# Kernel tuning notes

Hardware: AMD Instinct MI355X
Metric: run time of the kernel (lower is better)

The kernel has to match this reference:

```python
import jax, jax.numpy as jnp
import numpy as np

N, C, H, W = 8, 256, 128, 128
HD = 256          # hidden_depth
FC, FS, CS = 8, 2, 8  # heads_count, fold_size, center_size
EPS_GN = 1e-5


def setup_inputs() -> dict:
    key = jax.random.key(0)
    ks = jax.random.split(key, 8)
    d = {
        'x': jax.random.normal(ks[0], (N, C, H, W), jnp.float32),
        'proj_w': jax.random.normal(ks[1], (2 * HD, C), jnp.float32) * 0.02,
        'proj_b': jnp.zeros((2 * HD,), jnp.float32),
        'merge_w': jax.random.normal(ks[2], (C, HD), jnp.float32) * 0.02,
        'merge_b': jnp.zeros((C,), jnp.float32),
        'alpha': jnp.ones((1,), jnp.float32),
        'beta': jnp.zeros((1,), jnp.float32),
        'g0_w': jnp.ones((C,), jnp.float32),
        'g0_b': jnp.zeros((C,), jnp.float32),
        'mlp_w0': jax.random.normal(ks[3], (2 * C, 2 * C), jnp.float32) * 0.02,
        'mlp_b0': jnp.zeros((2 * C,), jnp.float32),
        'mlp_w1': jax.random.normal(ks[4], (2 * C, C), jnp.float32) * 0.02,
        'mlp_b1': jnp.zeros((C,), jnp.float32),
        'g1_w': jnp.ones((C,), jnp.float32),
        'g1_b': jnp.zeros((C,), jnp.float32),
        'layer_scale': jnp.full((C,), 1e-5, jnp.float32),
    }
    return d


def _group_norm1(x, w, b):
    # GroupNorm(1, C): normalize over (C,H,W) per sample, per-channel affine
    mu = x.mean(axis=(1, 2, 3), keepdims=True)
    var = ((x - mu) ** 2).mean(axis=(1, 2, 3), keepdims=True)
    xn = (x - mu) * jax.lax.rsqrt(var + EPS_GN)
    return xn * w[None, :, None, None] + b[None, :, None, None]


def _l2norm(v):
    return v / jnp.maximum(jnp.linalg.norm(v, axis=-1, keepdims=True), 1e-12)


def _local_cluster(x, proj_w, proj_b, merge_w, merge_b, alpha, beta):
    n = x.shape[0]
    # 1x1 conv proj: C -> 2*HD
    y = jnp.einsum('nchw,oc->nohw', x, proj_w) + proj_b[None, :, None, None]
    c = y.shape[1] // FC              # per-head channels (2*HD/FC)
    h, w = H // FS, W // FS
    # 'n (fc c) (fh h) (fw w) -> (n fc fh fw) c h w'
    y = y.reshape(n, FC, c, FS, h, FS, w).transpose(0, 1, 3, 5, 2, 4, 6)
    y = y.reshape(n * FC * FS * FS, c, h, w)
    m = y.shape[0]
    # adaptive avg pool to CSxCS (h,w divisible by CS -> uniform pooling)
    center = y.reshape(m, c, CS, h // CS, CS, w // CS).mean(axis=(3, 5))
    L, s = h * w, CS * CS
    yf = y.reshape(m, c, L).transpose(0, 2, 1)       # [m, L, c]
    cf = center.reshape(m, c, s).transpose(0, 2, 1)  # [m, s, c]
    cv = c // 2
    x_point, x_value = yf[..., :cv], yf[..., cv:]
    c_point, c_value = cf[..., :cv], cf[..., cv:]
    sim = jnp.einsum('mlc,msc->mls', _l2norm(x_point), _l2norm(c_point))
    sim = jax.nn.sigmoid(alpha * sim + beta)         # [m, L, s]
    vals = sim.max(axis=2)                           # [m, L]
    idx = sim.argmax(axis=2) + s * jnp.arange(m)[:, None]
    vals = vals.reshape(-1)
    idx = idx.reshape(-1)
    xv = x_value.reshape(-1, cv)
    cvv = c_value.reshape(-1, cv)
    xv_aug = jnp.concatenate([xv, jnp.ones((xv.shape[0], 1), xv.dtype)], axis=1)
    cv_aug = jnp.concatenate([cvv, jnp.ones((cvv.shape[0], 1), cvv.dtype)], axis=1)
    # scatter-add weighted points into centers
    nc = cv_aug.at[idx].add(vals[:, None] * xv_aug)
    nc = nc[:, :-1] / nc[:, -1:]
    # gather back
    nx = vals[:, None] * nc[idx]                     # [m*L, cv]
    # '(n fc fh fw h w) c -> n (fc c) (fh h) (fw w)'
    nx = nx.reshape(n, FC, FS, FS, h, w, cv).transpose(0, 1, 6, 2, 4, 3, 5)
    nx = nx.reshape(n, FC * cv, H, W)                # [n, HD, H, W]
    return jnp.einsum('nchw,oc->nohw', nx, merge_w) + merge_b[None, :, None, None]


def reference(x, proj_w, proj_b, merge_w, merge_b, alpha, beta, g0_w, g0_b,
              mlp_w0, mlp_b0, mlp_w1, mlp_b1, g1_w, g1_b, layer_scale):
    new_x = _local_cluster(x, proj_w, proj_b, merge_w, merge_b, alpha, beta)
    new_x = _group_norm1(new_x, g0_w, g0_b)
    t = jnp.concatenate([x, new_x], axis=1)          # [n, 2C, H, W]
    t = t.transpose(0, 2, 3, 1)                      # NHWC
    t = jax.nn.gelu(t @ mlp_w0 + mlp_b0, approximate=False)
    t = t @ mlp_w1 + mlp_b1
    t = t.transpose(0, 3, 1, 2)                      # NCHW
    t = _group_norm1(t, g1_w, g1_b)
    t = t * layer_scale[None, :, None, None]
    return t + x
```

## Files before the change

### kernel.cpp

```cpp
#include <hip/hip_runtime.h>
#include <math.h>

#define PIX   16384
#define NB    8
#define CIN   256

typedef __attribute__((ext_vector_type(8))) short    short8;
typedef __attribute__((ext_vector_type(4))) float    f32x4;
typedef __attribute__((ext_vector_type(4))) unsigned short us4;
typedef __attribute__((ext_vector_type(8))) unsigned short us8;

__device__ __forceinline__ float bf2f(unsigned short h) {
  return __uint_as_float(((unsigned int)h) << 16);
}
__device__ __forceinline__ unsigned short f2bf(float f) {
  unsigned int u = __float_as_uint(f);
  return (unsigned short)((u + 0x7FFFu + ((u >> 16) & 1u)) >> 16);
}
__device__ __forceinline__ float gelu_f(float v) {
  return 0.5f * v * (1.f + erff(v * 0.70710678118654752f));
}

__global__ void zero_kernel(float* p, int n) {
  int i = blockIdx.x * blockDim.x + threadIdx.x;
  if (i < n) p[i] = 0.f;
}

__global__ void prep_weights(const float* __restrict__ pw_f, const float* __restrict__ mw_f,
                             const float* __restrict__ w0, const float* __restrict__ w1,
                             unsigned short* __restrict__ pw, unsigned short* __restrict__ mw,
                             unsigned short* __restrict__ w0t, unsigned short* __restrict__ w1t) {
  const int S1 = 512 * 256, S2 = 256 * 256, S3 = 512 * 512, S4 = 256 * 512;
  int i = blockIdx.x * 256 + threadIdx.x;
  if (i < S1) { pw[i] = f2bf(pw_f[i]); return; }
  i -= S1;
  if (i < S2) { mw[i] = f2bf(mw_f[i]); return; }
  i -= S2;
  if (i < S3) { int o = i >> 9, k = i & 511; w0t[i] = f2bf(w0[k * 512 + o]); return; }
  i -= S3;
  if (i < S4) { int o = i >> 9, k = i & 511; w1t[i] = f2bf(w1[k * 256 + o]); }
}

__global__ __launch_bounds__(256) void x_to_nhwc(const float* __restrict__ x,
                                                 unsigned short* __restrict__ xT) {
  __shared__ float tile[64][65];
  const int t = threadIdx.x;
  const int p0 = blockIdx.x * 64, c0 = blockIdx.y * 64, n = blockIdx.z;
#pragma unroll
  for (int i = 0; i < 4; i++) {
    const int c = i * 16 + (t >> 4);
    const float4 v = *(const float4*)(x + ((size_t)(n * 256 + c0 + c) << 14) + p0 + (t & 15) * 4);
    tile[c][(t & 15) * 4]     = v.x;
    tile[c][(t & 15) * 4 + 1] = v.y;
    tile[c][(t & 15) * 4 + 2] = v.z;
    tile[c][(t & 15) * 4 + 3] = v.w;
  }
  __syncthreads();
#pragma unroll
  for (int i = 0; i < 4; i++) {
    const int pp = i * 16 + (t >> 4);
    const int cl = (t & 15) * 4;
    us4 o;
    o.x = f2bf(tile[cl][pp]); o.y = f2bf(tile[cl + 1][pp]);
    o.z = f2bf(tile[cl + 2][pp]); o.w = f2bf(tile[cl + 3][pp]);
    *(us4*)&xT[(((size_t)n << 14) + p0 + pp) * 256 + c0 + cl] = o;
  }
}

template<bool CONCAT, bool GELU>
__global__ __launch_bounds__(256, 2) void mfma_gemm(
    const unsigned short* __restrict__ A, const float* __restrict__ bias,
    const unsigned short* __restrict__ B1, const unsigned short* __restrict__ B2,
    unsigned short* __restrict__ Y, int M, int K, int K1) {
  __shared__ unsigned short As[8192];
  __shared__ unsigned short Bs[8192];
  const int t = threadIdx.x;
  const int lane = t & 63, w = t >> 6;
  const int quad = lane >> 4, l16 = lane & 15;
  const int p0 = blockIdx.x * 128, m0 = blockIdx.y * 128;
  const int n = blockIdx.z;
  const int wm = w & 1, wn = w >> 1;
  const int K2 = K - K1;

  f32x4 acc[4][4];
#pragma unroll
  for (int im = 0; im < 4; im++)
#pragma unroll
    for (int in = 0; in < 4; in++) acc[im][in] = (f32x4)0.f;

  for (int k0 = 0; k0 < K; k0 += 64) {
    __syncthreads();
#pragma unroll
    for (int i = 0; i < 4; i++) {
      const int c = (w << 2) | i;
      const int tm = c >> 1, kk = c & 1;
      const int krow = k0 + kk * 32 + quad * 8;
      const unsigned short* ga = A + (size_t)(m0 + tm * 16 + l16) * K + krow;
      __builtin_amdgcn_global_load_lds((const __attribute__((address_space(1))) void*)ga,
          (__attribute__((address_space(3))) void*)&As[c * 512], 16, 0, 0);
      const int prow = p0 + tm * 16 + l16;
      const unsigned short* gb;
      if (!CONCAT || krow < K1)
        gb = B1 + ((((size_t)n << 14) + prow) * (size_t)K1) + krow;
      else
        gb = B2 + ((((size_t)n << 14) + prow) * (size_t)K2) + (krow - K1);
      __builtin_amdgcn_global_load_lds((const __attribute__((address_space(1))) void*)gb,
          (__attribute__((address_space(3))) void*)&Bs[c * 512], 16, 0, 0);
    }
    __syncthreads();
#pragma unroll
    for (int kk = 0; kk < 2; kk++) {
      short8 af[4], bfr[4];
#pragma unroll
      for (int im = 0; im < 4; im++)
        af[im] = *(const short8*)&As[(((wm * 4 + im) * 2 + kk) * 64 + lane) * 8];
#pragma unroll
      for (int in = 0; in < 4; in++)
        bfr[in] = *(const short8*)&Bs[(((wn * 4 + in) * 2 + kk) * 64 + lane) * 8];
#pragma unroll
      for (int im = 0; im < 4; im++)
#pragma unroll
        for (int in = 0; in < 4; in++)
          acc[im][in] = __builtin_amdgcn_mfma_f32_16x16x32_bf16(af[im], bfr[in], acc[im][in], 0, 0, 0);
    }
  }

  const size_t nb = ((size_t)n << 14);
#pragma unroll
  for (int im = 0; im < 4; im++) {
    const int om = m0 + (wm * 4 + im) * 16 + quad * 4;
    const f32x4 bv = *(const f32x4*)(bias + om);
#pragma unroll
    for (int in = 0; in < 4; in++) {
      const int p = p0 + (wn * 4 + in) * 16 + l16;
      float v0 = acc[im][in].x + bv.x;
      float v1 = acc[im][in].y + bv.y;
      float v2 = acc[im][in].z + bv.z;
      float v3 = acc[im][in].w + bv.w;
      if (GELU) { v0 = gelu_f(v0); v1 = gelu_f(v1); v2 = gelu_f(v2); v3 = gelu_f(v3); }
      us4 o4;
      o4.x = f2bf(v0); o4.y = f2bf(v1); o4.z = f2bf(v2); o4.w = f2bf(v3);
      *(us4*)&Y[(nb + p) * M + om] = o4;
    }
  }
}

__global__ __launch_bounds__(256) void cluster_kernel(
    const unsigned short* __restrict__ y, const float* __restrict__ alpha_p,
    const float* __restrict__ beta_p, unsigned short* __restrict__ nx) {
  const int m = blockIdx.x;
  const int n = m >> 5, f = (m >> 2) & 7, s1 = (m >> 1) & 1, s2 = m & 1;
  const int t = threadIdx.x;
  const float alpha = alpha_p[0], beta = beta_p[0];

  __shared__ float cs[64][68];
  __shared__ float cpn[64][36];
  __shared__ float acc[64][33];
  __shared__ float svals[4096];
  __shared__ unsigned char sbest[4096];

  const size_t nbase = ((size_t)n << 14);
  const int prow0 = s1 * 64, pcol0 = s2 * 64;
  const int ch0 = f * 64;

  {
    const int b = t >> 2, g = t & 3;
    const int pr0 = prow0 + (b >> 3) * 8, pc0 = pcol0 + (b & 7) * 8;
    float a16[16];
#pragma unroll
    for (int j = 0; j < 16; j++) a16[j] = 0.f;
#pragma unroll 1
    for (int r = 0; r < 8; r++) {
#pragma unroll
      for (int cc = 0; cc < 8; cc++) {
        const int p = (pr0 + r) * 128 + pc0 + cc;
        const unsigned short* yp = y + (nbase + p) * 512 + ch0 + g * 16;
        const us8 v0 = *(const us8*)yp;
        const us8 v1 = *(const us8*)(yp + 8);
#pragma unroll
        for (int j = 0; j < 8; j++) { a16[j] += bf2f(v0[j]); a16[8 + j] += bf2f(v1[j]); }
      }
    }
#pragma unroll
    for (int j = 0; j < 16; j++) cs[b][g * 16 + j] = a16[j] * (1.f / 64.f);
  }
  __syncthreads();

  if (t < 64) {
    const int b = t;
    float s = 0.f;
#pragma unroll
    for (int cc = 0; cc < 32; cc++) { float v = cs[b][cc]; s = fmaf(v, v, s); }
    float inv = 1.f / fmaxf(sqrtf(s), 1e-12f);
#pragma unroll
    for (int cc = 0; cc < 32; cc++) cpn[b][cc] = cs[b][cc] * inv;
#pragma unroll
    for (int q = 0; q < 32; q++) acc[b][q] = cs[b][32 + q];
    acc[b][32] = 1.f;
  }
  __syncthreads();

#pragma unroll 1
  for (int g = 0; g < 8; g++) {
    const int la = g * 512 + t;
    const int lb = la + 256;
    const int pa = (prow0 + (la >> 6)) * 128 + pcol0 + (la & 63);
    const int pb = (prow0 + (lb >> 6)) * 128 + pcol0 + (lb & 63);
    const unsigned short* ya = y + (nbase + pa) * 512 + ch0;
    const unsigned short* yb = y + (nbase + pb) * 512 + ch0;
    float xpa[32], xpb[32];
#pragma unroll
    for (int q8 = 0; q8 < 4; q8++) {
      const us8 va = *(const us8*)(ya + q8 * 8);
      const us8 vb = *(const us8*)(yb + q8 * 8);
#pragma unroll
      for (int j = 0; j < 8; j++) { xpa[q8 * 8 + j] = bf2f(va[j]); xpb[q8 * 8 + j] = bf2f(vb[j]); }
    }
    float na = 0.f, nbv = 0.f;
#pragma unroll
    for (int cc = 0; cc < 32; cc++) {
      na = fmaf(xpa[cc], xpa[cc], na);
      nbv = fmaf(xpb[cc], xpb[cc], nbv);
    }
    const float inva = 1.f / fmaxf(sqrtf(na), 1e-12f);
    const float invb = 1.f / fmaxf(sqrtf(nbv), 1e-12f);
    float zma = -1e30f, zmb = -1e30f;
    int bba = 0, bbb = 0;
    for (int b = 0; b < 64; b++) {
      float da = 0.f, db = 0.f;
#pragma unroll
      for (int c4 = 0; c4 < 32; c4 += 4) {
        const float4 cp = *(const float4*)&cpn[b][c4];
        da = fmaf(xpa[c4], cp.x, da); da = fmaf(xpa[c4 + 1], cp.y, da);
        da = fmaf(xpa[c4 + 2], cp.z, da); da = fmaf(xpa[c4 + 3], cp.w, da);
        db = fmaf(xpb[c4], cp.x, db); db = fmaf(xpb[c4 + 1], cp.y, db);
        db = fmaf(xpb[c4 + 2], cp.z, db); db = fmaf(xpb[c4 + 3], cp.w, db);
      }
      const float za = fmaf(alpha, da * inva, beta);
      const float zb = fmaf(alpha, db * invb, beta);
      if (za > zma) { zma = za; bba = b; }
      if (zb > zmb) { zmb = zb; bbb = b; }
    }
    const float va = 1.f / (1.f + __expf(-zma));
    const float vb = 1.f / (1.f + __expf(-zmb));
    svals[la] = va; sbest[la] = (unsigned char)bba;
    svals[lb] = vb; sbest[lb] = (unsigned char)bbb;
#pragma unroll
    for (int q8 = 0; q8 < 4; q8++) {
      const us8 wa = *(const us8*)(ya + 32 + q8 * 8);
      const us8 wb = *(const us8*)(yb + 32 + q8 * 8);
#pragma unroll
      for (int j = 0; j < 8; j++) {
        atomicAdd(&acc[bba][q8 * 8 + j], va * bf2f(wa[j]));
        atomicAdd(&acc[bbb][q8 * 8 + j], vb * bf2f(wb[j]));
      }
    }
    atomicAdd(&acc[bba][32], va);
    atomicAdd(&acc[bbb][32], vb);
  }
  __syncthreads();

  for (int idx = t; idx < 2048; idx += 256) {
    const int b = idx >> 5, q = idx & 31;
    acc[b][q] = acc[b][q] / acc[b][32];
  }
  __syncthreads();

#pragma unroll 1
  for (int i = 0; i < 16; i++) {
    const int l = i * 256 + t;
    const int p = (prow0 + (l >> 6)) * 128 + pcol0 + (l & 63);
    const float v = svals[l];
    const int b = sbest[l];
    unsigned short* nr = nx + (nbase + p) * 256 + f * 32;
#pragma unroll
    for (int q8 = 0; q8 < 4; q8++) {
      us8 o;
#pragma unroll
      for (int j = 0; j < 8; j++) o[j] = f2bf(v * acc[b][q8 * 8 + j]);
      *(us8*)&nr[q8 * 8] = o;
    }
  }
}

__global__ __launch_bounds__(256) void gn_reduce_bf16(const unsigned short* __restrict__ v,
                                                      float* __restrict__ sums) {
  const int n = blockIdx.y;
  const us8* base = (const us8*)(v + ((size_t)n << 22));
  float s = 0.f, s2 = 0.f;
  for (int i = blockIdx.x * 256 + threadIdx.x; i < (1 << 19); i += 64 * 256) {
    const us8 x = base[i];
#pragma unroll
    for (int j = 0; j < 8; j++) {
      const float f = bf2f(x[j]);
      s += f;
      s2 = fmaf(f, f, s2);
    }
  }
  for (int off = 32; off > 0; off >>= 1) {
    s += __shfl_down(s, off);
    s2 += __shfl_down(s2, off);
  }
  __shared__ float ws1[4], ws2[4];
  const int wid = threadIdx.x >> 6, lanei = threadIdx.x & 63;
  if (lanei == 0) { ws1[wid] = s; ws2[wid] = s2; }
  __syncthreads();
  if (threadIdx.x == 0) {
    atomicAdd(&sums[2 * n],     ws1[0] + ws1[1] + ws1[2] + ws1[3]);
    atomicAdd(&sums[2 * n + 1], ws2[0] + ws2[1] + ws2[2] + ws2[3]);
  }
}

__global__ __launch_bounds__(256) void gn0_affine(unsigned short* __restrict__ v,
                                                  const float* __restrict__ sums,
                                                  const float* __restrict__ g0w,
                                                  const float* __restrict__ g0b) {
  const int i = blockIdx.x * 256 + threadIdx.x;
  const int n = i >> 19;
  const int cb = (i & 31) * 8;
  const float cntinv = 1.f / (float)(CIN * PIX);
  const float mu = sums[2 * n] * cntinv;
  const float var = sums[2 * n + 1] * cntinv - mu * mu;
  const float rs = rsqrtf(var + 1e-5f);
  us8* p = (us8*)v + i;
  const us8 x = *p;
  us8 o;
#pragma unroll
  for (int j = 0; j < 8; j++) {
    const float a = rs * g0w[cb + j];
    const float b = g0b[cb + j] - mu * a;
    o[j] = f2bf(fmaf(bf2f(x[j]), a, b));
  }
  *p = o;
}

__global__ __launch_bounds__(256) void final_transpose(
    const unsigned short* __restrict__ u, const float* __restrict__ x,
    const float* __restrict__ sums, const float* __restrict__ g1w,
    const float* __restrict__ g1b, const float* __restrict__ lsc,
    float* __restrict__ out) {
  __shared__ float tile[64][68];
  const int t = threadIdx.x;
  const int p0 = blockIdx.x * 64, c0 = blockIdx.y * 64, n = blockIdx.z;
  {
    const int pl = t >> 2, g = t & 3;
    const unsigned short* up = u + ((((size_t)n << 14) + p0 + pl) << 8) + c0 + g * 16;
    const us8 v0 = *(const us8*)up;
    const us8 v1 = *(const us8*)(up + 8);
#pragma unroll
    for (int j = 0; j < 8; j++) {
      tile[pl][g * 16 + j] = bf2f(v0[j]);
      tile[pl][g * 16 + 8 + j] = bf2f(v1[j]);
    }
  }
  __syncthreads();
  {
    const int cl = t >> 2, g = t & 3;
    const int c = c0 + cl;
    const float cntinv = 1.f / (float)(CIN * PIX);
    const float mu = sums[2 * n] * cntinv;
    const float var = sums[2 * n + 1] * cntinv - mu * mu;
    const float rs = rsqrtf(var + 1e-5f);
    const float gw = rs * g1w[c] * lsc[c];
    const float gb = (g1b[c] - mu * rs * g1w[c]) * lsc[c];
    const size_t rowb = ((size_t)(n * 256 + c) << 14) + p0 + g * 16;
#pragma unroll
    for (int q = 0; q < 4; q++) {
      const float4 xv = *(const float4*)(x + rowb + q * 4);
      float4 o;
      o.x = fmaf(tile[g * 16 + q * 4][cl], gw, gb) + xv.x;
      o.y = fmaf(tile[g * 16 + q * 4 + 1][cl], gw, gb) + xv.y;
      o.z = fmaf(tile[g * 16 + q * 4 + 2][cl], gw, gb) + xv.z;
      o.w = fmaf(tile[g * 16 + q * 4 + 3][cl], gw, gb) + xv.w;
      *(float4*)(out + rowb + q * 4) = o;
    }
  }
}

extern "C" void kernel_launch(void* const* d_in, const int* in_sizes, int n_in,
                              void* d_out, int out_size, void* d_ws, size_t ws_size,
                              hipStream_t stream) {
  const float* x       = (const float*)d_in[0];
  const float* proj_w  = (const float*)d_in[1];
  const float* proj_b  = (const float*)d_in[2];
  const float* merge_w = (const float*)d_in[3];
  const float* merge_b = (const float*)d_in[4];
  const float* alpha   = (const float*)d_in[5];
  const float* beta    = (const float*)d_in[6];
  const float* g0w     = (const float*)d_in[7];
  const float* g0b     = (const float*)d_in[8];
  const float* w0      = (const float*)d_in[9];
  const float* b0      = (const float*)d_in[10];
  const float* w1      = (const float*)d_in[11];
  const float* b1      = (const float*)d_in[12];
  const float* g1w     = (const float*)d_in[13];
  const float* g1b     = (const float*)d_in[14];
  const float* lsc     = (const float*)d_in[15];
  float* out = (float*)d_out;

  unsigned short* wsu = (unsigned short*)d_ws;
  unsigned short* xT  = wsu;
  unsigned short* y   = xT + (size_t)33554432;
  unsigned short* nx  = y + (size_t)67108864;
  unsigned short* pw  = nx + (size_t)33554432;
  unsigned short* mw  = pw + 131072;
  unsigned short* w0t = mw + 65536;
  unsigned short* w1t = w0t + 262144;
  float* sums = (float*)(w1t + 131072);
  unsigned short* newx = (unsigned short*)d_out;

  zero_kernel<<<1, 64, 0, stream>>>(sums, 32);
  prep_weights<<<2304, 256, 0, stream>>>(proj_w, merge_w, w0, w1, pw, mw, w0t, w1t);
  x_to_nhwc<<<dim3(256, 4, NB), 256, 0, stream>>>(x, xT);

  mfma_gemm<false, false><<<dim3(128, 4, NB), 256, 0, stream>>>(
      pw, proj_b, xT, nullptr, y, 512, 256, 256);

  cluster_kernel<<<256, 256, 0, stream>>>(y, alpha, beta, nx);

  mfma_gemm<false, false><<<dim3(128, 2, NB), 256, 0, stream>>>(
      mw, merge_b, nx, nullptr, newx, 256, 256, 256);

  gn_reduce_bf16<<<dim3(64, NB), 256, 0, stream>>>(newx, sums);
  gn0_affine<<<16384, 256, 0, stream>>>(newx, sums, g0w, g0b);

  mfma_gemm<true, true><<<dim3(128, 4, NB), 256, 0, stream>>>(
      w0t, b0, xT, newx, y, 512, 512, 256);

  mfma_gemm<false, false><<<dim3(128, 2, NB), 256, 0, stream>>>(
      w1t, b1, y, nullptr, nx, 256, 512, 512);

  gn_reduce_bf16<<<dim3(64, NB), 256, 0, stream>>>(nx, sums + 16);
  final_transpose<<<dim3(256, 4, NB), 256, 0, stream>>>(
      nx, x, sums + 16, g1w, g1b, lsc, out);
}
```

Before: 1.081 ms.

## Fuse GroupNorm stats into GEMM epilogues, fold GN0 into weights, MFMA clustering

GroupNorm sum and sum-of-squares are now accumulated in the merge and MLP-out GEMM epilogues, which removes the separate reduction passes. The GN0 affine is folded into per-sample scaled copies of w0 plus an effective bias, so the elementwise normalize pass over newx goes away. The cluster kernel moves to 1024-thread blocks and computes point-to-center similarities with bf16 MFMA and wave shuffles for the argmax, replacing the scalar dot-product loop. The trade-offs are bf16 rounding of normalized centers and scaled weights, per-sample weight copies, and more LDS atomic contention.

```diff
diff --git a/kernel.cpp b/kernel.cpp
--- a/kernel.cpp
+++ b/kernel.cpp
@@ -67,13 +67,15 @@
   }
 }
 
-template<bool CONCAT, bool GELU>
+template<bool CONCAT, bool GELU, bool STATS>
 __global__ __launch_bounds__(256, 2) void mfma_gemm(
     const unsigned short* __restrict__ A, const float* __restrict__ bias,
     const unsigned short* __restrict__ B1, const unsigned short* __restrict__ B2,
-    unsigned short* __restrict__ Y, int M, int K, int K1) {
+    unsigned short* __restrict__ Y, int M, int K, int K1,
+    int astride, int bstride, float* __restrict__ sums) {
   __shared__ unsigned short As[8192];
   __shared__ unsigned short Bs[8192];
+  __shared__ float r1[4], r2[4];
   const int t = threadIdx.x;
   const int lane = t & 63, w = t >> 6;
   const int quad = lane >> 4, l16 = lane & 15;
@@ -81,6 +83,8 @@
   const int n = blockIdx.z;
   const int wm = w & 1, wn = w >> 1;
   const int K2 = K - K1;
+
+  A += (size_t)n * astride;
 
   f32x4 acc[4][4];
 #pragma unroll
@@ -126,10 +130,11 @@
   }
 
   const size_t nb = ((size_t)n << 14);
+  float s = 0.f, s2 = 0.f;
 #pragma unroll
   for (int im = 0; im < 4; im++) {
     const int om = m0 + (wm * 4 + im) * 16 + quad * 4;
-    const f32x4 bv = *(const f32x4*)(bias + om);
+    const f32x4 bv = *(const f32x4*)(bias + (size_t)n * bstride + om);
 #pragma unroll
     for (int in = 0; in < 4; in++) {
       const int p = p0 + (wn * 4 + in) * 16 + l16;
@@ -138,24 +143,44 @@
       float v2 = acc[im][in].z + bv.z;
       float v3 = acc[im][in].w + bv.w;
       if (GELU) { v0 = gelu_f(v0); v1 = gelu_f(v1); v2 = gelu_f(v2); v3 = gelu_f(v3); }
+      if (STATS) {
+        s += (v0 + v1) + (v2 + v3);
+        s2 = fmaf(v0, v0, s2); s2 = fmaf(v1, v1, s2);
+        s2 = fmaf(v2, v2, s2); s2 = fmaf(v3, v3, s2);
+      }
       us4 o4;
       o4.x = f2bf(v0); o4.y = f2bf(v1); o4.z = f2bf(v2); o4.w = f2bf(v3);
       *(us4*)&Y[(nb + p) * M + om] = o4;
     }
   }
-}
-
-__global__ __launch_bounds__(256) void cluster_kernel(
+  if (STATS) {
+#pragma unroll
+    for (int off = 32; off > 0; off >>= 1) {
+      s += __shfl_down(s, off);
+      s2 += __shfl_down(s2, off);
+    }
+    if (lane == 0) { r1[w] = s; r2[w] = s2; }
+    __syncthreads();
+    if (t == 0) {
+      atomicAdd(&sums[2 * n],     (r1[0] + r1[1]) + (r1[2] + r1[3]));
+      atomicAdd(&sums[2 * n + 1], (r2[0] + r2[1]) + (r2[2] + r2[3]));
+    }
+  }
+}
+
+__global__ __launch_bounds__(1024) void cluster_kernel(
     const unsigned short* __restrict__ y, const float* __restrict__ alpha_p,
     const float* __restrict__ beta_p, unsigned short* __restrict__ nx) {
   const int m = blockIdx.x;
   const int n = m >> 5, f = (m >> 2) & 7, s1 = (m >> 1) & 1, s2 = m & 1;
   const int t = threadIdx.x;
+  const int wave = t >> 6, lane = t & 63;
+  const int quad = lane >> 4, l16 = lane & 15;
   const float alpha = alpha_p[0], beta = beta_p[0];
 
   __shared__ float cs[64][68];
-  __shared__ float cpn[64][36];
-  __shared__ float acc[64][33];
+  __shared__ unsigned short cpnh[64][32];
+  __shared__ float accv[64][36];
   __shared__ float svals[4096];
   __shared__ unsigned char sbest[4096];
 
@@ -164,25 +189,19 @@
   const int ch0 = f * 64;
 
   {
-    const int b = t >> 2, g = t & 3;
+    const int b = t >> 4, g = t & 15;
     const int pr0 = prow0 + (b >> 3) * 8, pc0 = pcol0 + (b & 7) * 8;
-    float a16[16];
-#pragma unroll
-    for (int j = 0; j < 16; j++) a16[j] = 0.f;
+    float a4[4] = {0.f, 0.f, 0.f, 0.f};
 #pragma unroll 1
     for (int r = 0; r < 8; r++) {
 #pragma unroll
       for (int cc = 0; cc < 8; cc++) {
-        const int p = (pr0 + r) * 128 + pc0 + cc;
-        const unsigned short* yp = y + (nbase + p) * 512 + ch0 + g * 16;
-        const us8 v0 = *(const us8*)yp;
-        const us8 v1 = *(const us8*)(yp + 8);
-#pragma unroll
-        for (int j = 0; j < 8; j++) { a16[j] += bf2f(v0[j]); a16[8 + j] += bf2f(v1[j]); }
+        const us4 v = *(const us4*)(y + (nbase + (size_t)(pr0 + r) * 128 + pc0 + cc) * 512 + ch0 + g * 4);
+        a4[0] += bf2f(v.x); a4[1] += bf2f(v.y); a4[2] += bf2f(v.z); a4[3] += bf2f(v.w);
       }
     }
 #pragma unroll
-    for (int j = 0; j < 16; j++) cs[b][g * 16 + j] = a16[j] * (1.f / 64.f);
+    for (int j = 0; j < 4; j++) cs[b][g * 4 + j] = a4[j] * (1.f / 64.f);
   }
   __syncthreads();
 
@@ -191,84 +210,90 @@
     float s = 0.f;
 #pragma unroll
     for (int cc = 0; cc < 32; cc++) { float v = cs[b][cc]; s = fmaf(v, v, s); }
-    float inv = 1.f / fmaxf(sqrtf(s), 1e-12f);
-#pragma unroll
-    for (int cc = 0; cc < 32; cc++) cpn[b][cc] = cs[b][cc] * inv;
-#pragma unroll
-    for (int q = 0; q < 32; q++) acc[b][q] = cs[b][32 + q];
-    acc[b][32] = 1.f;
+    const float inv = 1.f / fmaxf(sqrtf(s), 1e-12f);
+#pragma unroll
+    for (int cc = 0; cc < 32; cc++) cpnh[b][cc] = f2bf(cs[b][cc] * inv);
+#pragma unroll
+    for (int q = 0; q < 32; q++) accv[b][q] = cs[b][32 + q];
+    accv[b][32] = 1.f;
   }
   __syncthreads();
 
 #pragma unroll 1
-  for (int g = 0; g < 8; g++) {
-    const int la = g * 512 + t;
-    const int lb = la + 256;
-    const int pa = (prow0 + (la >> 6)) * 128 + pcol0 + (la & 63);
-    const int pb = (prow0 + (lb >> 6)) * 128 + pcol0 + (lb & 63);
-    const unsigned short* ya = y + (nbase + pa) * 512 + ch0;
-    const unsigned short* yb = y + (nbase + pb) * 512 + ch0;
-    float xpa[32], xpb[32];
-#pragma unroll
-    for (int q8 = 0; q8 < 4; q8++) {
-      const us8 va = *(const us8*)(ya + q8 * 8);
-      const us8 vb = *(const us8*)(yb + q8 * 8);
-#pragma unroll
-      for (int j = 0; j < 8; j++) { xpa[q8 * 8 + j] = bf2f(va[j]); xpb[q8 * 8 + j] = bf2f(vb[j]); }
-    }
-    float na = 0.f, nbv = 0.f;
-#pragma unroll
-    for (int cc = 0; cc < 32; cc++) {
-      na = fmaf(xpa[cc], xpa[cc], na);
-      nbv = fmaf(xpb[cc], xpb[cc], nbv);
-    }
-    const float inva = 1.f / fmaxf(sqrtf(na), 1e-12f);
-    const float invb = 1.f / fmaxf(sqrtf(nbv), 1e-12f);
-    float zma = -1e30f, zmb = -1e30f;
-    int bba = 0, bbb = 0;
-    for (int b = 0; b < 64; b++) {
-      float da = 0.f, db = 0.f;
-#pragma unroll
-      for (int c4 = 0; c4 < 32; c4 += 4) {
-        const float4 cp = *(const float4*)&cpn[b][c4];
-        da = fmaf(xpa[c4], cp.x, da); da = fmaf(xpa[c4 + 1], cp.y, da);
-        da = fmaf(xpa[c4 + 2], cp.z, da); da = fmaf(xpa[c4 + 3], cp.w, da);
-        db = fmaf(xpb[c4], cp.x, db); db = fmaf(xpb[c4 + 1], cp.y, db);
-        db = fmaf(xpb[c4 + 2], cp.z, db); db = fmaf(xpb[c4 + 3], cp.w, db);
+  for (int tile = 0; tile < 16; tile++) {
+    const int pidx = wave * 256 + tile * 16;
+    const int pix = (prow0 + (pidx >> 6)) * 128 + pcol0 + (pidx & 63) + l16;
+    const unsigned short* yp = y + (nbase + pix) * 512 + ch0;
+    const short8 apt = *(const short8*)(yp + quad * 8);
+    const short8 avl = *(const short8*)(yp + 32 + quad * 8);
+
+    float nrm = 0.f;
+#pragma unroll
+    for (int j = 0; j < 8; j++) {
+      const float fv = bf2f((unsigned short)apt[j]);
+      nrm = fmaf(fv, fv, nrm);
+    }
+    nrm += __shfl_xor(nrm, 16);
+    nrm += __shfl_xor(nrm, 32);
+    const float inva = 1.f / fmaxf(sqrtf(nrm), 1e-12f);
+
+    f32x4 d[4];
+#pragma unroll
+    for (int g = 0; g < 4; g++) {
+      const short8 bfr = *(const short8*)&cpnh[g * 16 + l16][quad * 8];
+      d[g] = __builtin_amdgcn_mfma_f32_16x16x32_bf16(apt, bfr, (f32x4)0.f, 0, 0, 0);
+    }
+
+    float bv[4]; int bi[4];
+#pragma unroll
+    for (int r = 0; r < 4; r++) {
+      bv[r] = d[0][r]; bi[r] = l16;
+#pragma unroll
+      for (int g = 1; g < 4; g++) {
+        const float c = d[g][r];
+        if (c > bv[r]) { bv[r] = c; bi[r] = g * 16 + l16; }
       }
-      const float za = fmaf(alpha, da * inva, beta);
-      const float zb = fmaf(alpha, db * invb, beta);
-      if (za > zma) { zma = za; bba = b; }
-      if (zb > zmb) { zmb = zb; bbb = b; }
-    }
-    const float va = 1.f / (1.f + __expf(-zma));
-    const float vb = 1.f / (1.f + __expf(-zmb));
-    svals[la] = va; sbest[la] = (unsigned char)bba;
-    svals[lb] = vb; sbest[lb] = (unsigned char)bbb;
-#pragma unroll
-    for (int q8 = 0; q8 < 4; q8++) {
-      const us8 wa = *(const us8*)(ya + 32 + q8 * 8);
-      const us8 wb = *(const us8*)(yb + 32 + q8 * 8);
-#pragma unroll
-      for (int j = 0; j < 8; j++) {
-        atomicAdd(&acc[bba][q8 * 8 + j], va * bf2f(wa[j]));
-        atomicAdd(&acc[bbb][q8 * 8 + j], vb * bf2f(wb[j]));
+    }
+#pragma unroll
+    for (int r = 0; r < 4; r++) {
+#pragma unroll
+      for (int msk = 1; msk < 16; msk <<= 1) {
+        const float v2 = __shfl_xor(bv[r], msk);
+        const int   i2 = __shfl_xor(bi[r], msk);
+        if (v2 > bv[r] || (v2 == bv[r] && i2 < bi[r])) { bv[r] = v2; bi[r] = i2; }
       }
     }
-    atomicAdd(&acc[bba][32], va);
-    atomicAdd(&acc[bbb][32], vb);
-  }
-  __syncthreads();
-
-  for (int idx = t; idx < 2048; idx += 256) {
-    const int b = idx >> 5, q = idx & 31;
-    acc[b][q] = acc[b][q] / acc[b][32];
-  }
-  __syncthreads();
-
-#pragma unroll 1
-  for (int i = 0; i < 16; i++) {
-    const int l = i * 256 + t;
+    const float rv01 = (l16 & 1) ? bv[1] : bv[0];
+    const float rv23 = (l16 & 1) ? bv[3] : bv[2];
+    const float rowv = (l16 & 2) ? rv23 : rv01;
+    const int   ri01 = (l16 & 1) ? bi[1] : bi[0];
+    const int   ri23 = (l16 & 1) ? bi[3] : bi[2];
+    const int   rowi = (l16 & 2) ? ri23 : ri01;
+    const int sl4 = (((l16 >> 2) << 4) | (l16 & 3)) << 2;
+    const float dot = __int_as_float(__builtin_amdgcn_ds_bpermute(sl4, __float_as_int(rowv)));
+    const int   idx = __builtin_amdgcn_ds_bpermute(sl4, rowi);
+
+    const float val = 1.f / (1.f + __expf(-fmaf(alpha, dot * inva, beta)));
+    if (quad == 0) {
+      svals[pidx + l16] = val;
+      sbest[pidx + l16] = (unsigned char)idx;
+    }
+#pragma unroll
+    for (int j = 0; j < 8; j++)
+      atomicAdd(&accv[idx][quad * 8 + j], val * bf2f((unsigned short)avl[j]));
+    if (quad == 0) atomicAdd(&accv[idx][32], val);
+  }
+  __syncthreads();
+
+  for (int i = t; i < 2048; i += 1024) {
+    const int b = i >> 5, q = i & 31;
+    accv[b][q] = accv[b][q] / accv[b][32];
+  }
+  __syncthreads();
+
+#pragma unroll
+  for (int i = 0; i < 4; i++) {
+    const int l = i * 1024 + t;
     const int p = (prow0 + (l >> 6)) * 128 + pcol0 + (l & 63);
     const float v = svals[l];
     const int b = sbest[l];
@@ -277,61 +302,45 @@
     for (int q8 = 0; q8 < 4; q8++) {
       us8 o;
 #pragma unroll
-      for (int j = 0; j < 8; j++) o[j] = f2bf(v * acc[b][q8 * 8 + j]);
+      for (int j = 0; j < 8; j++) o[j] = f2bf(v * accv[b][q8 * 8 + j]);
       *(us8*)&nr[q8 * 8] = o;
     }
   }
 }
 
-__global__ __launch_bounds__(256) void gn_reduce_bf16(const unsigned short* __restrict__ v,
-                                                      float* __restrict__ sums) {
-  const int n = blockIdx.y;
-  const us8* base = (const us8*)(v + ((size_t)n << 22));
-  float s = 0.f, s2 = 0.f;
-  for (int i = blockIdx.x * 256 + threadIdx.x; i < (1 << 19); i += 64 * 256) {
-    const us8 x = base[i];
-#pragma unroll
-    for (int j = 0; j < 8; j++) {
-      const float f = bf2f(x[j]);
-      s += f;
-      s2 = fmaf(f, f, s2);
-    }
-  }
-  for (int off = 32; off > 0; off >>= 1) {
-    s += __shfl_down(s, off);
-    s2 += __shfl_down(s2, off);
-  }
-  __shared__ float ws1[4], ws2[4];
-  const int wid = threadIdx.x >> 6, lanei = threadIdx.x & 63;
-  if (lanei == 0) { ws1[wid] = s; ws2[wid] = s2; }
-  __syncthreads();
-  if (threadIdx.x == 0) {
-    atomicAdd(&sums[2 * n],     ws1[0] + ws1[1] + ws1[2] + ws1[3]);
-    atomicAdd(&sums[2 * n + 1], ws2[0] + ws2[1] + ws2[2] + ws2[3]);
-  }
-}
-
-__global__ __launch_bounds__(256) void gn0_affine(unsigned short* __restrict__ v,
-                                                  const float* __restrict__ sums,
-                                                  const float* __restrict__ g0w,
-                                                  const float* __restrict__ g0b) {
-  const int i = blockIdx.x * 256 + threadIdx.x;
-  const int n = i >> 19;
-  const int cb = (i & 31) * 8;
+__global__ void gn_finalize0(const float* __restrict__ sums, const float* __restrict__ g0w,
+                             const float* __restrict__ g0b, float* __restrict__ scl,
+                             float* __restrict__ bia) {
+  const int n = blockIdx.x, c = threadIdx.x;
   const float cntinv = 1.f / (float)(CIN * PIX);
   const float mu = sums[2 * n] * cntinv;
   const float var = sums[2 * n + 1] * cntinv - mu * mu;
   const float rs = rsqrtf(var + 1e-5f);
-  us8* p = (us8*)v + i;
-  const us8 x = *p;
-  us8 o;
-#pragma unroll
-  for (int j = 0; j < 8; j++) {
-    const float a = rs * g0w[cb + j];
-    const float b = g0b[cb + j] - mu * a;
-    o[j] = f2bf(fmaf(bf2f(x[j]), a, b));
-  }
-  *p = o;
+  const float a = rs * g0w[c];
+  scl[n * 256 + c] = a;
+  bia[n * 256 + c] = g0b[c] - mu * a;
+}
+
+__global__ void w0_scale(const unsigned short* __restrict__ w0t,
+                         const float* __restrict__ scl, unsigned short* __restrict__ w0s) {
+  const int n = blockIdx.y;
+  const int i = blockIdx.x * 256 + threadIdx.x;
+  const int k = i & 511;
+  unsigned short v = w0t[i];
+  if (k >= 256) v = f2bf(bf2f(v) * scl[n * 256 + k - 256]);
+  w0s[(size_t)n * 262144 + i] = v;
+}
+
+__global__ void b0_eff(const unsigned short* __restrict__ w0t, const float* __restrict__ b0,
+                       const float* __restrict__ bia, float* __restrict__ b0e) {
+  const int n = blockIdx.y;
+  const int o = blockIdx.x * 256 + threadIdx.x;
+  float s = b0[o];
+  const unsigned short* wr = w0t + (size_t)o * 512 + 256;
+  const float* br = bia + n * 256;
+#pragma unroll 4
+  for (int k = 0; k < 256; k++) s = fmaf(bf2f(wr[k]), br[k], s);
+  b0e[n * 512 + o] = s;
 }
 
 __global__ __launch_bounds__(256) void final_transpose(
@@ -406,31 +415,35 @@
   unsigned short* mw  = pw + 131072;
   unsigned short* w0t = mw + 65536;
   unsigned short* w1t = w0t + 262144;
-  float* sums = (float*)(w1t + 131072);
+  unsigned short* w0s = w1t + 131072;
+  float* sums = (float*)(w0s + (size_t)2097152);
+  float* scl0 = sums + 32;
+  float* bia0 = scl0 + 2048;
+  float* b0e  = bia0 + 2048;
   unsigned short* newx = (unsigned short*)d_out;
 
   zero_kernel<<<1, 64, 0, stream>>>(sums, 32);
   prep_weights<<<2304, 256, 0, stream>>>(proj_w, merge_w, w0, w1, pw, mw, w0t, w1t);
   x_to_nhwc<<<dim3(256, 4, NB), 256, 0, stream>>>(x, xT);
 
-  mfma_gemm<false, false><<<dim3(128, 4, NB), 256, 0, stream>>>(
-      pw, proj_b, xT, nullptr, y, 512, 256, 256);
-
-  cluster_kernel<<<256, 256, 0, stream>>>(y, alpha, beta, nx);
-
-  mfma_gemm<false, false><<<dim3(128, 2, NB), 256, 0, stream>>>(
-      mw, merge_b, nx, nullptr, newx, 256, 256, 256);
-
-  gn_reduce_bf16<<<dim3(64, NB), 256, 0, stream>>>(newx, sums);
-  gn0_affine<<<16384, 256, 0, stream>>>(newx, sums, g0w, g0b);
-
-  mfma_gemm<true, true><<<dim3(128, 4, NB), 256, 0, stream>>>(
-      w0t, b0, xT, newx, y, 512, 512, 256);
-
-  mfma_gemm<false, false><<<dim3(128, 2, NB), 256, 0, stream>>>(
-      w1t, b1, y, nullptr, nx, 256, 512, 512);
-
-  gn_reduce_bf16<<<dim3(64, NB), 256, 0, stream>>>(nx, sums + 16);
+  mfma_gemm<false, false, false><<<dim3(128, 4, NB), 256, 0, stream>>>(
+      pw, proj_b, xT, nullptr, y, 512, 256, 256, 0, 0, nullptr);
+
+  cluster_kernel<<<256, 1024, 0, stream>>>(y, alpha, beta, nx);
+
+  mfma_gemm<false, false, true><<<dim3(128, 2, NB), 256, 0, stream>>>(
+      mw, merge_b, nx, nullptr, newx, 256, 256, 256, 0, 0, sums);
+
+  gn_finalize0<<<NB, 256, 0, stream>>>(sums, g0w, g0b, scl0, bia0);
+  w0_scale<<<dim3(1024, NB), 256, 0, stream>>>(w0t, scl0, w0s);
+  b0_eff<<<dim3(2, NB), 256, 0, stream>>>(w0t, b0, bia0, b0e);
+
+  mfma_gemm<true, true, false><<<dim3(128, 4, NB), 256, 0, stream>>>(
+      w0s, b0e, xT, newx, y, 512, 512, 256, 262144, 512, nullptr);
+
+  mfma_gemm<false, false, true><<<dim3(128, 2, NB), 256, 0, stream>>>(
+      w1t, b1, y, nullptr, nx, 256, 512, 512, 0, 0, sums + 16);
+
   final_transpose<<<dim3(256, 4, NB), 256, 0, stream>>>(
       nx, x, sums + 16, g1w, g1b, lsc, out);
 }
```

Measured after the change: 1.006 ms. 6.9% less time.
